# Performance work log

Hardware: AMD Instinct MI355X
Metric: run time of the kernel (lower is better)

## Reference

```python
import jax, jax.numpy as jnp
import numpy as np

B, S, D, DK = 8, 2048, 768, 214
DROPOUT_P = 0.1


def setup_inputs() -> dict:
    key = jax.random.key(0)
    ks = jax.random.split(key, 11)
    x1 = jax.random.normal(ks[0], (B, S, D), jnp.float32)
    x2 = jax.random.normal(ks[1], (B, S, D), jnp.float32)
    x3 = jax.random.normal(ks[2], (B, S, D), jnp.float32)
    Wq = jax.random.normal(ks[3], (DK, D), jnp.float32) * (1.0 / np.sqrt(D))
    bq = jax.random.normal(ks[4], (DK,), jnp.float32) * 0.01
    Wk = jax.random.normal(ks[5], (DK, D), jnp.float32) * (1.0 / np.sqrt(D))
    bk = jax.random.normal(ks[6], (DK,), jnp.float32) * 0.01
    Wv = jax.random.normal(ks[7], (D, D), jnp.float32) * (1.0 / np.sqrt(D))
    bv = jax.random.normal(ks[8], (D,), jnp.float32) * 0.01
    # full-tensor elementwise divisor: uniform(0,1) + 1, as in the source
    inv_scale = jax.random.uniform(ks[9], (S, S), jnp.float32) + 1.0
    # deterministic inverted-dropout mask, keep prob = 1 - p
    keep = 1.0 - DROPOUT_P
    dropout_mask = (jax.random.uniform(ks[10], (B, S, S)) < keep).astype(jnp.float32) / keep
    return dict(x1=x1, x2=x2, x3=x3, Wq=Wq, bq=bq, Wk=Wk, bk=bk,
                Wv=Wv, bv=bv, inv_scale=inv_scale, dropout_mask=dropout_mask)


def reference(x1, x2, x3, Wq, bq, Wk, bk, Wv, bv, inv_scale, dropout_mask):
    q = jnp.einsum('bsd,kd->bsk', x1, Wq) + bq          # [B,S,DK]
    k = jnp.einsum('bsd,kd->bsk', x2, Wk) + bk          # [B,S,DK]
    v = jnp.einsum('bsd,ed->bse', x3, Wv) + bv          # [B,S,D]
    attn = jnp.einsum('bsk,btk->bst', q, k)             # [B,S,S]
    scaled = attn / inv_scale                           # elementwise full-tensor divisor
    p = jax.nn.softmax(scaled, axis=-1) * dropout_mask  # softmax + inverted dropout
    return jnp.einsum('bst,btd->bsd', p, v)             # [B,S,D]
```

## Files before the change

### kernel.cpp

```cpp
#include <hip/hip_runtime.h>
#include <hip/hip_bf16.h>

typedef unsigned short ushort;
typedef unsigned long long u64;
typedef short bf16x8 __attribute__((ext_vector_type(8)));
typedef _Float16 f16x8 __attribute__((ext_vector_type(8)));
typedef float f32x4 __attribute__((ext_vector_type(4)));

#define NB 8
#define SS 2048
#define DD 768
#define DKV 214
#define DKP 224
#define WROWS 256
#define MSHIFT 40.0f

__device__ __forceinline__ float bf2f(ushort u) {
  union { unsigned int i; float f; } v; v.i = ((unsigned int)u) << 16; return v.f;
}
__device__ __forceinline__ ushort f2bf(float f) {
  union { float f; unsigned int i; } v; v.f = f;
  unsigned int x = v.i;
  return (ushort)((x + 0x7fffu + ((x >> 16) & 1u)) >> 16);
}
__device__ __forceinline__ ushort f2h(float f) {
  union { _Float16 h; ushort u; } cv; cv.h = (_Float16)f; return cv.u;
}
__device__ __forceinline__ bf16x8 cvt8v(f32x4 a, f32x4 b) {
  bf16x8 r;
#pragma unroll
  for (int j = 0; j < 4; ++j) { r[j] = (short)f2bf(a[j]); r[j + 4] = (short)f2bf(b[j]); }
  return r;
}
__device__ __forceinline__ f16x8 cvt8h(f32x4 a, f32x4 b) {
  f16x8 r;
#pragma unroll
  for (int j = 0; j < 4; ++j) { r[j] = (_Float16)a[j]; r[j + 4] = (_Float16)b[j]; }
  return r;
}
__device__ __forceinline__ void gload16(const void* g, void* l) {
  __builtin_amdgcn_global_load_lds(
      (const __attribute__((address_space(1))) void*)g,
      (__attribute__((address_space(3))) void*)l, 16, 0, 0);
}

__global__ __launch_bounds__(256)
void prep_all(const float* __restrict__ dmk, const float* __restrict__ Wq,
              const float* __restrict__ Wk, const float* __restrict__ Wv,
              u64* __restrict__ dbits, ushort* __restrict__ Wqp,
              ushort* __restrict__ Wkp, ushort* __restrict__ Wvb,
              float* __restrict__ Z)
{
  const int tid0 = blockIdx.x * 256 + threadIdx.x;
  const int stride = gridDim.x * 256;
  for (int i = tid0; i < NB * SS; i += stride) Z[i] = 0.f;
  const int NW = WROWS * DD;
  const int NV = DD * DD;
  for (int i = tid0; i < 2 * NW + NV; i += stride) {
    if (i < NW) {
      int r = i / DD, c = i % DD;
      float v = (r < DKV) ? Wq[i] : 0.f;
      Wqp[(c >> 5) * (WROWS * 32) + r * 32 + (c & 31)] = f2h(v);
    } else if (i < 2 * NW) {
      int j = i - NW;
      int r = j / DD, c = j % DD;
      float v = (r < DKV) ? Wk[j] : 0.f;
      Wkp[(c >> 5) * (WROWS * 32) + r * 32 + (c & 31)] = f2h(v);
    } else {
      int j = i - 2 * NW;
      int r = j / DD, c = j % DD;
      Wvb[(c >> 5) * (DD * 32) + r * 32 + (c & 31)] = f2bf(Wv[j]);
    }
  }
  const size_t nwords = (size_t)NB * SS * SS / 64;
  for (size_t wi = tid0; wi < nwords; wi += stride) {
    const f32x4* p = (const f32x4*)(dmk + wi * 64);
    u64 m = 0;
#pragma unroll
    for (int j = 0; j < 16; ++j) {
      f32x4 v = p[j];
#pragma unroll
      for (int q = 0; q < 4; ++q) m |= (v[q] > 0.5f) ? (1ull << (j * 4 + q)) : 0ull;
    }
    dbits[wi] = m;
  }
}

__global__ __launch_bounds__(256, 4)
void gemm_qk(const float* __restrict__ x1, const float* __restrict__ x2,
             const ushort* __restrict__ Wqp, const ushort* __restrict__ Wkp,
             const float* __restrict__ bq, const float* __restrict__ bk,
             ushort* __restrict__ Qp, ushort* __restrict__ Kp)
{
  const int m0 = blockIdx.x * 64;
  const int which = blockIdx.y >> 1;
  const int n0 = (blockIdx.y & 1) * 128;
  const int tid = threadIdx.x;
  const int w  = tid >> 6;
  const int l  = tid & 63;
  const int lr = l & 15;
  const int lh = l >> 4;

  const float*  A    = which ? x2 : x1;
  const ushort* Bw   = which ? Wkp : Wqp;
  const float*  bias = which ? bk : bq;
  ushort* Cp = which ? Kp : Qp;

  __shared__ __align__(16) char lds[2][128][64];

  const int srow = (w << 4) + (l >> 2);
  const size_t gc = (size_t)srow * 64 + (size_t)((((l & 3) ^ ((srow >> 1) & 3))) << 4);
  const char* gb = (const char*)Bw + (size_t)n0 * 64;

  const f32x4 fzero = {0.f, 0.f, 0.f, 0.f};
  f32x4 acc[8];
#pragma unroll
  for (int nt = 0; nt < 8; ++nt) acc[nt] = fzero;

  const float* arow = A + (size_t)(m0 + w * 16 + lr) * DD + lh * 8;

#define QKSTAGE(buf, kk) do {                                             \
    size_t ko = (size_t)(kk) * (WROWS * 64);                              \
    gload16(gb + ko + gc,        &lds[buf][w << 4][0]);                   \
    gload16(gb + ko + gc + 4096, &lds[buf][(w << 4) + 64][0]);            \
  } while (0)

  QKSTAGE(0, 0);
  f32x4 pa = *(const f32x4*)(arow);
  f32x4 pb = *(const f32x4*)(arow + 4);
  __syncthreads();

  for (int kk = 0; kk < 24; ++kk) {
    const int buf = kk & 1;
    if (kk < 23) QKSTAGE(buf ^ 1, kk + 1);
    f32x4 na = fzero, nb = fzero;
    if (kk < 23) {
      na = *(const f32x4*)(arow + (kk + 1) * 32);
      nb = *(const f32x4*)(arow + (kk + 1) * 32 + 4);
    }
    f16x8 af = cvt8h(pa, pb);
#pragma unroll
    for (int nt = 0; nt < 8; ++nt) {
      int br = nt * 16 + lr;
      int bo = (lh ^ ((br >> 1) & 3)) << 4;
      f16x8 wf = *(const f16x8*)&lds[buf][br][bo];
      acc[nt] = __builtin_amdgcn_mfma_f32_16x16x32_f16(af, wf, acc[nt], 0, 0, 0);
    }
    __syncthreads();
    pa = na; pb = nb;
  }
#undef QKSTAGE

#pragma unroll
  for (int nt = 0; nt < 8; ++nt) {
    int n = n0 + nt * 16 + lr;
    if (n >= DKP) continue;
    float bv = (n < DKV) ? bias[n] : 0.f;
#pragma unroll
    for (int r = 0; r < 4; ++r) {
      int m = m0 + w * 16 + lh * 4 + r;
      int bb = m >> 11, s = m & 2047;
      float val = (n < DKV) ? (acc[nt][r] + bv) : 0.f;
      Cp[((size_t)(bb * 7 + (n >> 5)) * SS + s) * 32 + (n & 31)] = f2h(val);
    }
  }
}

__global__ __launch_bounds__(256, 3)
void gemm_v(const float* __restrict__ A, const ushort* __restrict__ Bw,
            const float* __restrict__ bias, ushort* __restrict__ Vp)
{
  const int m0 = blockIdx.x * 64;
  const int n0 = blockIdx.y * 256;
  const int tid = threadIdx.x;
  const int w  = tid >> 6;
  const int l  = tid & 63;
  const int lr = l & 15;
  const int lh = l >> 4;

  __shared__ __align__(16) char smem[36864];
  typedef char VBuf[256][64];
  VBuf* stage = (VBuf*)smem;
  ushort (*lt)[72] = (ushort(*)[72])smem;

  const int srow = (w << 4) + (l >> 2);
  const size_t gc = (size_t)srow * 64 + (size_t)((((l & 3) ^ ((srow >> 1) & 3))) << 4);
  const char* gvw = (const char*)Bw + (size_t)n0 * 64;

  const f32x4 fzero = {0.f, 0.f, 0.f, 0.f};
  f32x4 acc[16];
#pragma unroll
  for (int nt = 0; nt < 16; ++nt) acc[nt] = fzero;

  const float* arow = A + (size_t)(m0 + w * 16 + lr) * DD + lh * 8;

#define VSTAGE(buf, kk) do {                                              \
    size_t ko = (size_t)(kk) * (DD * 64);                                 \
    gload16(gvw + ko + gc,         &stage[buf][w << 4][0]);               \
    gload16(gvw + ko + gc + 4096,  &stage[buf][(w << 4) + 64][0]);        \
    gload16(gvw + ko + gc + 8192,  &stage[buf][(w << 4) + 128][0]);       \
    gload16(gvw + ko + gc + 12288, &stage[buf][(w << 4) + 192][0]);       \
  } while (0)

  VSTAGE(0, 0);
  f32x4 pa = *(const f32x4*)(arow);
  f32x4 pb = *(const f32x4*)(arow + 4);
  __syncthreads();

  for (int kk = 0; kk < 24; ++kk) {
    const int buf = kk & 1;
    if (kk < 23) VSTAGE(buf ^ 1, kk + 1);
    f32x4 na = fzero, nb = fzero;
    if (kk < 23) {
      na = *(const f32x4*)(arow + (kk + 1) * 32);
      nb = *(const f32x4*)(arow + (kk + 1) * 32 + 4);
    }
    bf16x8 af = cvt8v(pa, pb);
#pragma unroll
    for (int nt = 0; nt < 16; ++nt) {
      int br = nt * 16 + lr;
      int bo = (lh ^ ((br >> 1) & 3)) << 4;
      bf16x8 bfr = *(const bf16x8*)&stage[buf][br][bo];
      acc[nt] = __builtin_amdgcn_mfma_f32_16x16x32_bf16(af, bfr, acc[nt], 0, 0, 0);
    }
    __syncthreads();
    pa = na; pb = nb;
  }
#undef VSTAGE

#pragma unroll
  for (int nt = 0; nt < 16; ++nt) {
    int nl = nt * 16 + lr;
    float bv = bias[n0 + nl];
#pragma unroll
    for (int r = 0; r < 4; ++r)
      lt[nl][w * 16 + lh * 4 + r] = f2bf(acc[nt][r] + bv);
  }
  __syncthreads();
  const int bb = m0 >> 11;
  const int s0 = m0 & 2047;
  for (int i = tid; i < 256 * 64; i += 256) {
    int nn = i >> 6, mm = i & 63;
    int d = n0 + nn, t = s0 + mm;
    Vp[((size_t)(bb * 64 + (t >> 5)) * DD + d) * 32 + (t & 31)] = lt[nn][mm];
  }
}

__global__ __launch_bounds__(512, 4)
void gemm_s(const ushort* __restrict__ Qp, const ushort* __restrict__ Kp,
            const float* __restrict__ isc, const u64* __restrict__ dbits,
            ushort* __restrict__ Pp, float* __restrict__ Z)
{
  const int bid = blockIdx.x;
  const int bb = bid & 7;
  const int tt = bid >> 3;
  const int m0 = (tt & 15) * 128;
  const int n0 = (tt >> 4) * 256;
  const int tid = threadIdx.x;
  const int w  = tid >> 6;
  const int l  = tid & 63;
  const int lr = l & 15;
  const int lh = l >> 4;
  const int wm = w & 1;
  const int wn = w >> 1;

  __shared__ __align__(16) char Qb[2][128][64];
  __shared__ __align__(16) char Kb[2][256][64];

  const int srow = (w << 4) + (l >> 2);
  const size_t gc = (size_t)srow * 64 + (size_t)((((l & 3) ^ ((srow >> 1) & 3))) << 4);

  const char* gq = (const char*)Qp + ((size_t)(bb * 7) * SS + m0) * 64;
  const char* gk = (const char*)Kp + ((size_t)(bb * 7) * SS + n0) * 64;

  const f32x4 fzero = {0.f, 0.f, 0.f, 0.f};
  f32x4 acc[4][4];
#pragma unroll
  for (int mf = 0; mf < 4; ++mf)
#pragma unroll
    for (int nf = 0; nf < 4; ++nf) acc[mf][nf] = fzero;

#define SSTAGE(buf, kk) do {                                            \
    size_t ko = (size_t)(kk) * (SS * 64);                               \
    gload16(gq + ko + gc,        &Qb[buf][w << 4][0]);                  \
    gload16(gk + ko + gc,        &Kb[buf][w << 4][0]);                  \
    gload16(gk + ko + gc + 8192, &Kb[buf][(w << 4) + 128][0]);          \
  } while (0)

  SSTAGE(0, 0);
  __syncthreads();
#pragma unroll 1
  for (int t = 0; t < 7; ++t) {
    const int buf = t & 1;
    if (t < 6) SSTAGE(buf ^ 1, t + 1);
    f16x8 bfr[4];
#pragma unroll
    for (int nf = 0; nf < 4; ++nf) {
      int br = wn * 64 + nf * 16 + lr;
      int bo = (lh ^ ((br >> 1) & 3)) << 4;
      bfr[nf] = *(const f16x8*)&Kb[buf][br][bo];
    }
#pragma unroll
    for (int mf = 0; mf < 4; ++mf) {
      int ar = wm * 64 + mf * 16 + lr;
      int ao = (lh ^ ((ar >> 1) & 3)) << 4;
      f16x8 af = *(const f16x8*)&Qb[buf][ar][ao];
#pragma unroll
      for (int nf = 0; nf < 4; ++nf)
        acc[mf][nf] = __builtin_amdgcn_mfma_f32_16x16x32_f16(af, bfr[nf], acc[mf][nf], 0, 0, 0);
    }
    __syncthreads();
  }
#undef SSTAGE

  const float KEEPR = 1.0f / 0.9f;
#pragma unroll
  for (int mf = 0; mf < 4; ++mf) {
#pragma unroll
    for (int r = 0; r < 4; ++r) {
      const int sr = m0 + wm * 64 + mf * 16 + lh * 4 + r;
      const u64 wbits = dbits[((size_t)bb * SS + sr) * (SS / 64) + (n0 >> 6) + wn];
      float z = 0.f;
#pragma unroll
      for (int nf = 0; nf < 4; ++nf) {
        const int tc = n0 + wn * 64 + nf * 16 + lr;
        float iv = isc[(size_t)sr * SS + tc];
        float sval = acc[mf][nf][r] * __builtin_amdgcn_rcpf(iv);
        float e = __expf(sval - MSHIFT);
        z += e;
        float pm = ((wbits >> (nf * 16 + lr)) & 1ull) ? (e * KEEPR) : 0.f;
        Pp[((size_t)(bb * 64 + (tc >> 5)) * SS + sr) * 32 + (tc & 31)] = f2bf(pm);
      }
#pragma unroll
      for (int off = 1; off < 16; off <<= 1) z += __shfl_xor(z, off);
      if (lr == 0) atomicAdd(&Z[bb * SS + sr], z);
    }
  }
}

__global__ __launch_bounds__(256, 4)
void gemm_pv(const ushort* __restrict__ Pp, const ushort* __restrict__ Vp,
             const float* __restrict__ Z, float* __restrict__ out)
{
  const int bid = blockIdx.x;
  const int bb = bid & 7;
  const int tt = bid >> 3;
  const int m_idx = tt / 6;
  const int n_idx = tt - m_idx * 6;
  const int m0 = m_idx * 128;
  const int n0 = n_idx * 128;
  const int tid = threadIdx.x;
  const int w  = tid >> 6;
  const int l  = tid & 63;
  const int lr = l & 15;
  const int lh = l >> 4;
  const int wm = w & 1;
  const int wn = w >> 1;

  __shared__ __align__(16) char Plb[2][128][64];
  __shared__ __align__(16) char Vlb[2][128][64];

  const int srow = (w << 4) + (l >> 2);
  const size_t gc = (size_t)srow * 64 + (size_t)((((l & 3) ^ ((srow >> 1) & 3))) << 4);

  const char* gpb = (const char*)Pp + ((size_t)(bb * 64) * SS + m0) * 64;
  const char* gvb = (const char*)Vp + ((size_t)(bb * 64) * DD + n0) * 64;

  const f32x4 fzero = {0.f, 0.f, 0.f, 0.f};
  f32x4 acc[4][4];
#pragma unroll
  for (int mf = 0; mf < 4; ++mf)
#pragma unroll
    for (int nf = 0; nf < 4; ++nf) acc[mf][nf] = fzero;

#define PVSTAGE(t) do {                                                   \
    size_t k0 = (size_t)(t) * 2;                                          \
    gload16(gpb + k0 * (SS * 64) + gc,              &Plb[0][w << 4][0]);  \
    gload16(gpb + k0 * (SS * 64) + gc + 4096,       &Plb[0][(w << 4) + 64][0]); \
    gload16(gpb + (k0 + 1) * (SS * 64) + gc,        &Plb[1][w << 4][0]);  \
    gload16(gpb + (k0 + 1) * (SS * 64) + gc + 4096, &Plb[1][(w << 4) + 64][0]); \
    gload16(gvb + k0 * (DD * 64) + gc,              &Vlb[0][w << 4][0]);  \
    gload16(gvb + k0 * (DD * 64) + gc + 4096,       &Vlb[0][(w << 4) + 64][0]); \
    gload16(gvb + (k0 + 1) * (DD * 64) + gc,        &Vlb[1][w << 4][0]);  \
    gload16(gvb + (k0 + 1) * (DD * 64) + gc + 4096, &Vlb[1][(w << 4) + 64][0]); \
  } while (0)

  PVSTAGE(0);
  __syncthreads();
#pragma unroll 1
  for (int t = 0; t < 32; ++t) {
#pragma unroll
    for (int pk = 0; pk < 2; ++pk) {
      bf16x8 bfr[4];
#pragma unroll
      for (int nf = 0; nf < 4; ++nf) {
        int br = wn * 64 + nf * 16 + lr;
        int bo = (lh ^ ((br >> 1) & 3)) << 4;
        bfr[nf] = *(const bf16x8*)&Vlb[pk][br][bo];
      }
#pragma unroll
      for (int mf = 0; mf < 4; ++mf) {
        int ar = wm * 64 + mf * 16 + lr;
        int ao = (lh ^ ((ar >> 1) & 3)) << 4;
        bf16x8 af = *(const bf16x8*)&Plb[pk][ar][ao];
#pragma unroll
        for (int nf = 0; nf < 4; ++nf)
          acc[mf][nf] = __builtin_amdgcn_mfma_f32_16x16x32_bf16(af, bfr[nf], acc[mf][nf], 0, 0, 0);
      }
    }
    __syncthreads();
    if (t < 31) {
      PVSTAGE(t + 1);
      __syncthreads();
    }
  }
#undef PVSTAGE

#pragma unroll
  for (int mf = 0; mf < 4; ++mf) {
#pragma unroll
    for (int r = 0; r < 4; ++r) {
      const int sr = m0 + wm * 64 + mf * 16 + lh * 4 + r;
      float rz = __builtin_amdgcn_rcpf(Z[bb * SS + sr]);
#pragma unroll
      for (int nf = 0; nf < 4; ++nf) {
        const int dc = n0 + wn * 64 + nf * 16 + lr;
        out[((size_t)bb * SS + sr) * DD + dc] = acc[mf][nf][r] * rz;
      }
    }
  }
}

extern "C" void kernel_launch(void* const* d_in, const int* in_sizes, int n_in,
                              void* d_out, int out_size, void* d_ws, size_t ws_size,
                              hipStream_t stream) {
  const float* x1  = (const float*)d_in[0];
  const float* x2  = (const float*)d_in[1];
  const float* x3  = (const float*)d_in[2];
  const float* Wq  = (const float*)d_in[3];
  const float* bq  = (const float*)d_in[4];
  const float* Wk  = (const float*)d_in[5];
  const float* bk  = (const float*)d_in[6];
  const float* Wv  = (const float*)d_in[7];
  const float* bv  = (const float*)d_in[8];
  const float* isc = (const float*)d_in[9];
  const float* dmk = (const float*)d_in[10];
  float* out = (float*)d_out;

  const size_t QKN = (size_t)NB * 7 * SS * 32;
  const size_t VPN = (size_t)NB * 64 * DD * 32;
  const size_t WN  = (size_t)WROWS * DD;
  const size_t NV  = (size_t)DD * DD;
  const size_t PPN = (size_t)NB * 64 * SS * 32;

  ushort* Qp  = (ushort*)d_ws;
  ushort* Kp  = Qp + QKN;
  ushort* Vp  = Kp + QKN;
  ushort* Wqp = Vp + VPN;
  ushort* Wkp = Wqp + WN;
  ushort* Wvb = Wkp + WN;
  ushort* Pp  = Wvb + NV;
  float*  Zb  = (float*)(Pp + PPN);
  u64*    dbits = (u64*)(Zb + NB * SS);

  dim3 blk(256);
  prep_all<<<dim3(2048), blk, 0, stream>>>(dmk, Wq, Wk, Wv, dbits, Wqp, Wkp, Wvb, Zb);
  gemm_qk<<<dim3(256, 4), blk, 0, stream>>>(x1, x2, Wqp, Wkp, bq, bk, Qp, Kp);
  gemm_v <<<dim3(256, 3), blk, 0, stream>>>(x3, Wvb, bv, Vp);
  gemm_s <<<dim3(1024), dim3(512), 0, stream>>>(Qp, Kp, isc, dbits, Pp, Zb);
  gemm_pv<<<dim3(768),  dim3(256), 0, stream>>>(Pp, Vp, Zb, out);
}
```

Before: 258.9 us.

## Pack dropout mask with wave ballots and widen QK GEMM tile to all columns

The dropout mask packing now reads coalesced float4 per lane and builds the bit words with wave ballots, which interleaves the bit layout. The score kernel's bit indexing is updated to match. The Q/K projection kernel now computes all 224 padded output columns per block, staging 256 weight rows instead of splitting N across two blocks. This stops the fp32 activations from being re-read by each split. In exchange it uses more accumulator registers and twice the shared memory per block.

```diff
diff --git a/kernel.cpp b/kernel.cpp
--- a/kernel.cpp
+++ b/kernel.cpp
@@ -72,17 +72,20 @@
       Wvb[(c >> 5) * (DD * 32) + r * 32 + (c & 31)] = f2bf(Wv[j]);
     }
   }
-  const size_t nwords = (size_t)NB * SS * SS / 64;
-  for (size_t wi = tid0; wi < nwords; wi += stride) {
-    const f32x4* p = (const f32x4*)(dmk + wi * 64);
-    u64 m = 0;
-#pragma unroll
-    for (int j = 0; j < 16; ++j) {
-      f32x4 v = p[j];
-#pragma unroll
-      for (int q = 0; q < 4; ++q) m |= (v[q] > 0.5f) ? (1ull << (j * 4 + q)) : 0ull;
-    }
-    dbits[wi] = m;
+  const int l = threadIdx.x & 63;
+  const int wv = tid0 >> 6;
+  const int nw = stride >> 6;
+  const size_t nchunks = (size_t)NB * SS * SS / 256;
+  for (size_t c = wv; c < nchunks; c += nw) {
+    f32x4 v = *(const f32x4*)(dmk + c * 256 + 4 * l);
+    u64 b0 = __ballot(v[0] > 0.5f);
+    u64 b1 = __ballot(v[1] > 0.5f);
+    u64 b2 = __ballot(v[2] > 0.5f);
+    u64 b3 = __ballot(v[3] > 0.5f);
+    if (l == 0) {
+      u64* d = dbits + c * 4;
+      d[0] = b0; d[1] = b1; d[2] = b2; d[3] = b3;
+    }
   }
 }
 
@@ -93,8 +96,7 @@
              ushort* __restrict__ Qp, ushort* __restrict__ Kp)
 {
   const int m0 = blockIdx.x * 64;
-  const int which = blockIdx.y >> 1;
-  const int n0 = (blockIdx.y & 1) * 128;
+  const int which = blockIdx.y;
   const int tid = threadIdx.x;
   const int w  = tid >> 6;
   const int l  = tid & 63;
@@ -106,23 +108,25 @@
   const float*  bias = which ? bk : bq;
   ushort* Cp = which ? Kp : Qp;
 
-  __shared__ __align__(16) char lds[2][128][64];
+  __shared__ __align__(16) char lds[2][256][64];
 
   const int srow = (w << 4) + (l >> 2);
   const size_t gc = (size_t)srow * 64 + (size_t)((((l & 3) ^ ((srow >> 1) & 3))) << 4);
-  const char* gb = (const char*)Bw + (size_t)n0 * 64;
+  const char* gb = (const char*)Bw;
 
   const f32x4 fzero = {0.f, 0.f, 0.f, 0.f};
-  f32x4 acc[8];
-#pragma unroll
-  for (int nt = 0; nt < 8; ++nt) acc[nt] = fzero;
+  f32x4 acc[14];
+#pragma unroll
+  for (int nt = 0; nt < 14; ++nt) acc[nt] = fzero;
 
   const float* arow = A + (size_t)(m0 + w * 16 + lr) * DD + lh * 8;
 
 #define QKSTAGE(buf, kk) do {                                             \
     size_t ko = (size_t)(kk) * (WROWS * 64);                              \
-    gload16(gb + ko + gc,        &lds[buf][w << 4][0]);                   \
-    gload16(gb + ko + gc + 4096, &lds[buf][(w << 4) + 64][0]);            \
+    gload16(gb + ko + gc,         &lds[buf][w << 4][0]);                  \
+    gload16(gb + ko + gc + 4096,  &lds[buf][(w << 4) + 64][0]);           \
+    gload16(gb + ko + gc + 8192,  &lds[buf][(w << 4) + 128][0]);          \
+    gload16(gb + ko + gc + 12288, &lds[buf][(w << 4) + 192][0]);          \
   } while (0)
 
   QKSTAGE(0, 0);
@@ -140,7 +144,7 @@
     }
     f16x8 af = cvt8h(pa, pb);
 #pragma unroll
-    for (int nt = 0; nt < 8; ++nt) {
+    for (int nt = 0; nt < 14; ++nt) {
       int br = nt * 16 + lr;
       int bo = (lh ^ ((br >> 1) & 3)) << 4;
       f16x8 wf = *(const f16x8*)&lds[buf][br][bo];
@@ -152,9 +156,8 @@
 #undef QKSTAGE
 
 #pragma unroll
-  for (int nt = 0; nt < 8; ++nt) {
-    int n = n0 + nt * 16 + lr;
-    if (n >= DKP) continue;
+  for (int nt = 0; nt < 14; ++nt) {
+    int n = nt * 16 + lr;
     float bv = (n < DKV) ? bias[n] : 0.f;
 #pragma unroll
     for (int r = 0; r < 4; ++r) {
@@ -319,7 +322,7 @@
 #pragma unroll
     for (int r = 0; r < 4; ++r) {
       const int sr = m0 + wm * 64 + mf * 16 + lh * 4 + r;
-      const u64 wbits = dbits[((size_t)bb * SS + sr) * (SS / 64) + (n0 >> 6) + wn];
+      const u64 wbits = dbits[((size_t)bb * SS + sr) * 32 + (n0 >> 6) + (lr & 3)];
       float z = 0.f;
 #pragma unroll
       for (int nf = 0; nf < 4; ++nf) {
@@ -328,7 +331,7 @@
         float sval = acc[mf][nf][r] * __builtin_amdgcn_rcpf(iv);
         float e = __expf(sval - MSHIFT);
         z += e;
-        float pm = ((wbits >> (nf * 16 + lr)) & 1ull) ? (e * KEEPR) : 0.f;
+        float pm = ((wbits >> (wn * 16 + nf * 4 + (lr >> 2))) & 1ull) ? (e * KEEPR) : 0.f;
         Pp[((size_t)(bb * 64 + (tc >> 5)) * SS + sr) * 32 + (tc & 31)] = f2bf(pm);
       }
 #pragma unroll
@@ -465,7 +468,7 @@
 
   dim3 blk(256);
   prep_all<<<dim3(2048), blk, 0, stream>>>(dmk, Wq, Wk, Wv, dbits, Wqp, Wkp, Wvb, Zb);
-  gemm_qk<<<dim3(256, 4), blk, 0, stream>>>(x1, x2, Wqp, Wkp, bq, bk, Qp, Kp);
+  gemm_qk<<<dim3(256, 2), blk, 0, stream>>>(x1, x2, Wqp, Wkp, bq, bk, Qp, Kp);
   gemm_v <<<dim3(256, 3), blk, 0, stream>>>(x3, Wvb, bv, Vp);
   gemm_s <<<dim3(1024), dim3(512), 0, stream>>>(Qp, Kp, isc, dbits, Pp, Zb);
   gemm_pv<<<dim3(768),  dim3(256), 0, stream>>>(Pp, Vp, Zb, out);
```

Result: faster. 237.2 us, median of 2 (-8.4%).
